# Optimization experiments

Measured on AMD Instinct MI355X. Metric: run time of the kernel, lower is better.

The kernel has to match this reference:

```python
import jax, jax.numpy as jnp
import numpy as np

NEG = -1e9
TAU = 1.0
N_SAMPLES = 5
SWEEP = (0.1, 0.5, 5)


def layer_norm(x, g, b, eps=1e-5):
    m = x.mean(-1, keepdims=True)
    v = x.var(-1, keepdims=True)
    return (x - m) / jnp.sqrt(v + eps) * g + b


def entmax15(z):
    # exact 1.5-entmax along last axis (Peters & Martins 2019 sort-based algorithm)
    z = z / 2.0
    zs = jnp.sort(z, axis=-1)[..., ::-1]               # descending
    T = z.shape[-1]
    kk = jnp.arange(1, T + 1, dtype=z.dtype)
    mean = jnp.cumsum(zs, -1) / kk
    mean_sq = jnp.cumsum(zs * zs, -1) / kk
    ss = kk * (mean_sq - mean * mean)
    delta = jnp.clip((1.0 - ss) / kk, 0.0)
    tau = mean - jnp.sqrt(delta)
    support = jnp.sum((tau <= zs).astype(jnp.int32), -1, keepdims=True)  # k_star
    tau_star = jnp.take_along_axis(tau, support - 1, axis=-1)
    return jnp.square(jnp.clip(z - tau_star, 0.0))


def stochastic_topk(key, scores, attn, k, tau, n_samples):
    # vectorized over samples AND batch rows with per-row variable k:
    # threshold = k-th largest perturbed score per row (ties measure-zero w/ gumbel)
    u = jax.random.uniform(key, (n_samples,) + scores.shape)
    noise = -jnp.log(-jnp.log(u + 1e-6) + 1e-6)
    pert = jnp.where(attn[None] == 0, NEG, scores[None] + noise * tau)  # [S,B,T]
    srt = jnp.sort(pert, -1)[..., ::-1]
    idx = jnp.broadcast_to((k - 1)[None, :, None], pert.shape[:2] + (1,))
    thr = jnp.take_along_axis(srt, idx, axis=-1)       # [S,B,1]
    h = (pert >= thr).astype(scores.dtype)
    return h.mean(0)                                   # [B,T]


def pool(tok, attn):
    # masked mean pooling (stand-in for sent_encoder.pool)
    return (tok * attn[..., None]).sum(1) / jnp.clip(attn.sum(1, keepdims=True), 1e-6)


def _forward(ids, embeddings, attn, ln_g, ln_b, W1, b1, W2, b2, emb_table):
    emb = embeddings * attn[..., None]
    h = jax.nn.gelu(layer_norm(emb, ln_g, ln_b) @ W1 + b1, approximate=False)
    scores = (h @ W2 + b2)[..., 0]                     # [B,T]
    scores = jnp.where(attn == 0, NEG, scores)

    tok = emb_table[ids]                               # stand-in token embeddings
    full_rep = jax.lax.stop_gradient(pool(tok, attn))  # torch.no_grad path

    T_eff = attn.sum(1)                                # [B]
    # g_soft is identical across the rho sweep in the original; hoisted here
    g_soft = entmax15(scores / TAU) * attn
    g_soft = g_soft / jnp.clip(g_soft.sum(1, keepdims=True), 1e-6)

    key = jax.random.key(42)
    rhos = np.linspace(*SWEEP)
    g_sweep, loss_sweep, rho_eff_sweep = [], [], []
    recon_sum = jnp.zeros((), embeddings.dtype)
    g = None
    for j, rho in enumerate(rhos):
        k = jnp.maximum((float(rho) * T_eff).astype(jnp.int32), 1)
        g_hard = stochastic_topk(jax.random.fold_in(key, j), scores, attn, k, TAU, N_SAMPLES)
        # straight-through: hard forward, soft (entmax) backward
        g = jax.lax.stop_gradient(g_hard) - jax.lax.stop_gradient(g_soft) + g_soft
        rho_eff_sweep.append(g.sum(1) / T_eff)
        eff_attn = attn * g
        pred_rep = pool(tok, eff_attn)
        l_r = jnp.mean(jnp.square(pred_rep - full_rep))  # recon_loss = MSE stand-in
        recon_sum = recon_sum + l_r
        g_sweep.append(g)
        loss_sweep.append(l_r)
    recon_avg = recon_sum / len(rhos)
    return g, jnp.stack(g_sweep), recon_avg, jnp.stack(loss_sweep), jnp.stack(rho_eff_sweep)


def setup_inputs() -> dict:
    key = jax.random.key(0)
    B, T, D, H, V = 8, 2048, 1024, 1365, 32000
    ks = jax.random.split(key, 8)
    return {
        "ids": jax.random.randint(ks[0], (B, T), 0, V),
        "embeddings": jax.random.normal(ks[1], (B, T, D), jnp.float32),
        "attn": jnp.ones((B, T), jnp.float32),
        "ln_g": jnp.ones((D,), jnp.float32),
        "ln_b": jnp.zeros((D,), jnp.float32),
        "W1": jax.random.normal(ks[2], (D, H), jnp.float32) * 0.02,
        "b1": jnp.zeros((H,), jnp.float32),
        "W2": jax.random.normal(ks[3], (H, 1), jnp.float32) * 0.02,
        "b2": jnp.zeros((1,), jnp.float32),
        "emb_table": jax.random.normal(ks[4], (V, D), jnp.float32) * 0.02,
    }


def reference(ids, embeddings, attn, ln_g, ln_b, W1, b1, W2, b2, emb_table):
    return _forward(ids, embeddings, attn, ln_g, ln_b, W1, b1, W2, b2, emb_table)
```

## Files before the change

kernel.cpp:

```cpp
#include <hip/hip_runtime.h>
#include <math.h>
#include <stdint.h>

#define B_ 8
#define T_ 2048
#define D_ 1024
#define H_ 1365
#define HPAD 1536
#define NTOK (B_*T_)
#define NSAMP 5
#define NRHO 5

typedef float  f32x4  __attribute__((ext_vector_type(4)));
typedef __bf16 bf16x8 __attribute__((ext_vector_type(8)));

#define WS_SCORES 0
#define WS_CNT    (WS_SCORES + NTOK*8)
#define WS_PREDW  (WS_CNT + NRHO*B_*T_*4)
#define WS_FULLW  (WS_PREDW + NRHO*B_*D_*8)
#define WS_SUMEFF (WS_FULLW + B_*D_*8)
#define WS_SUMATT (WS_SUMEFF + NRHO*B_*8)
#define WS_SUMG   (WS_SUMATT + B_*8)
#define WS_ZERO_BYTES (WS_SUMG + NRHO*B_*8)
#define WS_STATS  (WS_SUMG + NRHO*B_*8)
#define WS_W1THI  (WS_STATS + NTOK*8)
#define WS_W1TLO  (WS_W1THI + (size_t)HPAD*D_*2)
#define WS_AHI    (WS_W1TLO + (size_t)HPAD*D_*2)
#define WS_ALO    (WS_AHI + (size_t)NTOK*D_*2)
#define WS_FULL_END (WS_ALO + (size_t)NTOK*D_*2)

#define OUT_G      0
#define OUT_GSW    16384
#define OUT_RECON  98304
#define OUT_LOSS   98305
#define OUT_RHOEFF 98310

__device__ inline unsigned short f2bf(float x) {
    uint32_t u = __float_as_uint(x);
    return (unsigned short)((u + 0x7FFFu + ((u >> 16) & 1u)) >> 16);
}

__launch_bounds__(256)
__global__ void k_w1t(const float* __restrict__ W1, unsigned short* __restrict__ hi,
                      unsigned short* __restrict__ lo)
{
    __shared__ float tile[32][33];
    const int tid = threadIdx.x;
    const int bk = blockIdx.x & 31;
    const int bh = blockIdx.x >> 5;
    const int k0 = bk * 32, h0 = bh * 32;
    const int a = tid & 31, b = tid >> 5;
    #pragma unroll
    for (int i = 0; i < 4; ++i) {
        int k = k0 + b + i * 8;
        int h = h0 + a;
        tile[b + i*8][a] = (h < H_) ? W1[(size_t)k * H_ + h] : 0.0f;
    }
    __syncthreads();
    #pragma unroll
    for (int i = 0; i < 4; ++i) {
        int hrow = h0 + b + i * 8;
        int kcol = k0 + a;
        float v = tile[a][b + i*8];
        unsigned short hb = f2bf(v);
        float hf = __uint_as_float((uint32_t)hb << 16);
        unsigned short lb = f2bf(v - hf);
        size_t dst = (size_t)hrow * D_ + kcol;
        hi[dst] = hb; lo[dst] = lb;
    }
}

__launch_bounds__(256)
__global__ void k_asplit(const float* __restrict__ emb, const float* __restrict__ attn,
                         const float* __restrict__ ln_g, const float* __restrict__ ln_b,
                         unsigned short* __restrict__ ahi, unsigned short* __restrict__ alo)
{
    const int tid = threadIdx.x, l = tid & 63, w = tid >> 6;
    const int t0 = blockIdx.x * 64;
    for (int tk = w; tk < 64; tk += 4) {
        const int tg = t0 + tk;
        const float av = attn[tg];
        const float* row = emb + (size_t)tg * D_;
        float rv[16];
        double s1 = 0.0, s2 = 0.0;
        #pragma unroll
        for (int i = 0; i < 16; ++i) {
            rv[i] = row[i*64 + l];
            double x = (double)rv[i] * (double)av;
            s1 += x; s2 += x * x;
        }
        for (int m = 32; m; m >>= 1) { s1 += __shfl_xor(s1, m); s2 += __shfl_xor(s2, m); }
        double mean = s1 / (double)D_;
        double var  = s2 / (double)D_ - mean * mean;
        double inv  = 1.0 / sqrt(var + 1e-5);
        float sc  = (float)((double)av * inv);
        float nsh = -(float)(mean * inv);
        #pragma unroll
        for (int i = 0; i < 16; ++i) {
            int k = i * 64 + l;
            float t  = fmaf(rv[i], sc, nsh);
            float xn = fmaf(t, ln_g[k], ln_b[k]);
            unsigned short hb = f2bf(xn);
            float hf = __uint_as_float((uint32_t)hb << 16);
            size_t dst = (size_t)tg * D_ + k;
            ahi[dst] = hb;
            alo[dst] = f2bf(xn - hf);
        }
    }
}

__launch_bounds__(256)
__global__ void k_stats(const float* __restrict__ emb, const float* __restrict__ attn,
                        float2* __restrict__ stats)
{
    const int tid = threadIdx.x, l = tid & 63, w = tid >> 6;
    const int t0 = blockIdx.x * 64;
    for (int tk = w; tk < 64; tk += 4) {
        const int tg = t0 + tk;
        const float av = attn[tg];
        const float* row = emb + (size_t)tg * D_;
        double s1 = 0.0, s2 = 0.0;
        #pragma unroll
        for (int i = 0; i < D_/64; ++i) {
            double x = (double)row[i*64 + l] * (double)av;
            s1 += x; s2 += x * x;
        }
        for (int m = 32; m; m >>= 1) { s1 += __shfl_xor(s1, m); s2 += __shfl_xor(s2, m); }
        if (l == 0) {
            double mean = s1 / (double)D_;
            double var  = s2 / (double)D_ - mean * mean;
            double inv  = 1.0 / sqrt(var + 1e-5);
            stats[tg] = make_float2((float)((double)av * inv), (float)(mean * inv));
        }
    }
}

#define BUFU 24576
#define OFF_ALO 4096
#define OFF_BHI 8192
#define OFF_BLO 16384
#define KSTEPS 32

__device__ __forceinline__ void gll16(const unsigned short* g, unsigned short* l)
{
    __builtin_amdgcn_global_load_lds((const __attribute__((address_space(1))) void*)g,
                                     (__attribute__((address_space(3))) void*)l, 16, 0, 0);
}

__launch_bounds__(512, 2)
__global__ void k_scores8(const unsigned short* __restrict__ ahi,
                          const unsigned short* __restrict__ alo,
                          const unsigned short* __restrict__ w1thi,
                          const unsigned short* __restrict__ w1tlo,
                          const float* __restrict__ b1, const float* __restrict__ W2,
                          double* __restrict__ scores)
{
    __shared__ __align__(16) unsigned short smem[3*BUFU];

    const int tid = threadIdx.x;
    const int blk = blockIdx.x;
    const int lin = (blk & 7) * 96 + (blk >> 3);
    const int mm = lin / 6, hh = lin - mm * 6;
    const int t0 = mm * 128;
    const int h0 = hh * 256;

    const int l  = tid & 63, w = tid >> 6;
    const int wr = w >> 2, wcn = w & 3;
    const int lm = l & 15, lq = l >> 4;

    const int lrow  = l >> 2;
    const int lslot = (l & 3) ^ ((l >> 3) & 3);
    const unsigned short* sA_hi  = ahi   + (size_t)(t0 + w*16 + lrow) * D_ + lslot*8;
    const unsigned short* sA_lo  = alo   + (size_t)(t0 + w*16 + lrow) * D_ + lslot*8;
    const unsigned short* sB_hi0 = w1thi + (size_t)(h0 + w*32 + lrow) * D_ + lslot*8;
    const unsigned short* sB_hi1 = sB_hi0 + 16*D_;
    const unsigned short* sB_lo0 = w1tlo + (size_t)(h0 + w*32 + lrow) * D_ + lslot*8;
    const unsigned short* sB_lo1 = sB_lo0 + 16*D_;
    const int dAhi  = w*512,            dAlo  = OFF_ALO + w*512;
    const int dBhi0 = OFF_BHI + w*1024, dBhi1 = dBhi0 + 512;
    const int dBlo0 = OFF_BLO + w*1024, dBlo1 = dBlo0 + 512;

    const int sw8 = (lq ^ ((lm >> 1) & 3)) * 8;
    int offAh[4], offBh[4];
    #pragma unroll
    for (int r = 0; r < 4; ++r) offAh[r] = (wr*64 + r*16 + lm)*32 + sw8;
    #pragma unroll
    for (int c = 0; c < 4; ++c) offBh[c] = OFF_BHI + (wcn*64 + c*16 + lm)*32 + sw8;

    f32x4 acc[4][4];
    #pragma unroll
    for (int r = 0; r < 4; ++r)
        #pragma unroll
        for (int c = 0; c < 4; ++c) acc[r][c] = (f32x4){0.f, 0.f, 0.f, 0.f};

    gll16(sA_hi,       &smem[0*BUFU + dAhi]);
    gll16(sA_lo,       &smem[0*BUFU + dAlo]);
    gll16(sB_hi0,      &smem[0*BUFU + dBhi0]);
    gll16(sB_hi1,      &smem[0*BUFU + dBhi1]);
    gll16(sB_lo0,      &smem[0*BUFU + dBlo0]);
    gll16(sB_lo1,      &smem[0*BUFU + dBlo1]);
    gll16(sA_hi  + 32, &smem[1*BUFU + dAhi]);
    gll16(sA_lo  + 32, &smem[1*BUFU + dAlo]);
    gll16(sB_hi0 + 32, &smem[1*BUFU + dBhi0]);
    gll16(sB_hi1 + 32, &smem[1*BUFU + dBhi1]);
    gll16(sB_lo0 + 32, &smem[1*BUFU + dBlo0]);
    gll16(sB_lo1 + 32, &smem[1*BUFU + dBlo1]);
    asm volatile("s_waitcnt vmcnt(6)" ::: "memory");
    asm volatile("s_barrier" ::: "memory");

    int dbase = 0, ebase = 2*BUFU;
    #pragma unroll 1
    for (int t = 0; t < KSTEPS; ++t) {
        const int  stK = (t + 2) * 32;
        const bool st  = (t < KSTEPS - 2);
        bf16x8 ah[4], bh[4];
        #pragma unroll
        for (int r = 0; r < 4; ++r) ah[r] = *(const bf16x8*)&smem[dbase + offAh[r]];
        #pragma unroll
        for (int c = 0; c < 4; ++c) bh[c] = *(const bf16x8*)&smem[dbase + offBh[c]];
        if (st) { gll16(sA_hi + stK, &smem[ebase + dAhi]);
                  gll16(sA_lo + stK, &smem[ebase + dAlo]); }
        asm volatile("s_barrier" ::: "memory");
        asm volatile("s_waitcnt lgkmcnt(0)" ::: "memory");
        __builtin_amdgcn_sched_barrier(0);
        __builtin_amdgcn_s_setprio(1);
        #pragma unroll
        for (int r = 0; r < 4; ++r)
            #pragma unroll
            for (int c = 0; c < 4; ++c)
                acc[r][c] = __builtin_amdgcn_mfma_f32_16x16x32_bf16(ah[r], bh[c], acc[r][c], 0, 0, 0);
        __builtin_amdgcn_s_setprio(0);
        asm volatile("s_barrier" ::: "memory");
        bf16x8 bl[4];
        #pragma unroll
        for (int c = 0; c < 4; ++c) bl[c] = *(const bf16x8*)&smem[dbase + offBh[c] + (OFF_BLO - OFF_BHI)];
        if (st) { gll16(sB_hi0 + stK, &smem[ebase + dBhi0]);
                  gll16(sB_hi1 + stK, &smem[ebase + dBhi1]); }
        asm volatile("s_barrier" ::: "memory");
        asm volatile("s_waitcnt lgkmcnt(0)" ::: "memory");
        __builtin_amdgcn_sched_barrier(0);
        __builtin_amdgcn_s_setprio(1);
        #pragma unroll
        for (int r = 0; r < 4; ++r)
            #pragma unroll
            for (int c = 0; c < 4; ++c)
                acc[r][c] = __builtin_amdgcn_mfma_f32_16x16x32_bf16(ah[r], bl[c], acc[r][c], 0, 0, 0);
        __builtin_amdgcn_s_setprio(0);
        asm volatile("s_barrier" ::: "memory");
        bf16x8 al[4];
        #pragma unroll
        for (int r = 0; r < 4; ++r) al[r] = *(const bf16x8*)&smem[dbase + offAh[r] + OFF_ALO];
        if (st) { gll16(sB_lo0 + stK, &smem[ebase + dBlo0]);
                  gll16(sB_lo1 + stK, &smem[ebase + dBlo1]); }
        asm volatile("s_barrier" ::: "memory");
        asm volatile("s_waitcnt lgkmcnt(0)" ::: "memory");
        __builtin_amdgcn_sched_barrier(0);
        __builtin_amdgcn_s_setprio(1);
        #pragma unroll
        for (int r = 0; r < 4; ++r)
            #pragma unroll
            for (int c = 0; c < 4; ++c)
                acc[r][c] = __builtin_amdgcn_mfma_f32_16x16x32_bf16(al[r], bh[c], acc[r][c], 0, 0, 0);
        __builtin_amdgcn_s_setprio(0);
        if (st) asm volatile("s_waitcnt vmcnt(6)" ::: "memory");
        else    asm volatile("s_waitcnt vmcnt(0)" ::: "memory");
        asm volatile("s_barrier" ::: "memory");
        dbase = (dbase == 2*BUFU) ? 0 : dbase + BUFU;
        ebase = (ebase == 2*BUFU) ? 0 : ebase + BUFU;
    }

    float b1v[4], w2v[4];
    #pragma unroll
    for (int c = 0; c < 4; ++c) {
        int hg = h0 + wcn*64 + c*16 + lm;
        bool ok = (hg < H_);
        b1v[c] = ok ? b1[hg] : 0.0f;
        w2v[c] = ok ? W2[hg] : 0.0f;
    }
    const float is2 = 0.70710678118654752440f;
    #pragma unroll
    for (int r = 0; r < 4; ++r) {
        #pragma unroll
        for (int i = 0; i < 4; ++i) {
            float ps = 0.0f;
            #pragma unroll
            for (int c = 0; c < 4; ++c) {
                float z  = acc[r][c][i] + b1v[c];
                float gl = 0.5f * z * (1.0f + erff(z * is2));
                ps = fmaf(gl, w2v[c], ps);
            }
            double psd = (double)ps;
            psd += __shfl_xor(psd, 1);
            psd += __shfl_xor(psd, 2);
            psd += __shfl_xor(psd, 4);
            psd += __shfl_xor(psd, 8);
            if (lm == 0)
                atomicAdd(&scores[t0 + wr*64 + r*16 + lq*4 + i], psd);
        }
    }
}

__launch_bounds__(256)
__global__ void k_scores_fb(const float* __restrict__ emb, const float* __restrict__ ln_g,
                            const float* __restrict__ ln_b, const float2* __restrict__ stats,
                            const unsigned short* __restrict__ w1thi,
                            const unsigned short* __restrict__ w1tlo,
                            const float* __restrict__ b1, const float* __restrict__ W2,
                            double* __restrict__ scores)
{
    __shared__ __align__(16) unsigned short sAhi[128*40];
    __shared__ __align__(16) unsigned short sAlo[128*40];
    __shared__ __align__(16) unsigned short sBhi[128*40];
    __shared__ __align__(16) unsigned short sBlo[128*40];
    __shared__ float sS1[128], sS2[128];

    const int tid = threadIdx.x;
    const int blk = blockIdx.x;
    const int xcd = blk & 7, slot = blk >> 3;
    const int lin = xcd * 176 + slot;
    const int tt = lin / 11, hh = lin - tt * 11;
    const int t0 = tt * 128;
    const int h0 = hh * 128;

    if (tid < 128) {
        float2 st = stats[t0 + tid];
        sS1[tid] = st.x; sS2[tid] = st.y;
    }
    f32x4 acc[4][4];
    #pragma unroll
    for (int r = 0; r < 4; ++r)
        #pragma unroll
        for (int c = 0; c < 4; ++c) acc[r][c] = (f32x4){0.f, 0.f, 0.f, 0.f};
    const int l = tid & 63, w = tid >> 6;
    const int lm = l & 15, lq = l >> 4;
    const int wr = (w >> 1) * 64;
    const int wc = (w & 1) * 64;
    __syncthreads();

    for (int kc = 0; kc < D_; kc += 32) {
        #pragma unroll
        for (int r2 = 0; r2 < 2; ++r2) {
            int g = tid + r2 * 256;
            int row = g >> 2, oct = g & 3;
            size_t src = (size_t)(h0 + row) * D_ + kc + oct * 8;
            int dst = row * 40 + oct * 8;
            *(bf16x8*)&sBhi[dst] = *(const bf16x8*)&w1thi[src];
            *(bf16x8*)&sBlo[dst] = *(const bf16x8*)&w1tlo[src];
        }
        #pragma unroll
        for (int r2 = 0; r2 < 2; ++r2) {
            int g = tid + r2 * 256;
            int tk = g >> 2, oct = g & 3;
            int tg = t0 + tk, dg = kc + oct * 8;
            const float* ep = emb + (size_t)tg * D_ + dg;
            float s1 = sS1[tk], ns2 = -sS2[tk];
            union { unsigned short s[8]; bf16x8 v; } hi, lo;
            #pragma unroll
            for (int j = 0; j < 8; ++j) {
                float t  = fmaf(ep[j], s1, ns2);
                float xn = fmaf(t, ln_g[dg + j], ln_b[dg + j]);
                unsigned short hb = f2bf(xn);
                float hf = __uint_as_float((uint32_t)hb << 16);
                hi.s[j] = hb;
                lo.s[j] = f2bf(xn - hf);
            }
            int dst = tk * 40 + oct * 8;
            *(bf16x8*)&sAhi[dst] = hi.v;
            *(bf16x8*)&sAlo[dst] = lo.v;
        }
        __syncthreads();
        bf16x8 ah[4], al[4], bh[4], bl[4];
        #pragma unroll
        for (int r = 0; r < 4; ++r) {
            int off = (wr + r * 16 + lm) * 40 + lq * 8;
            ah[r] = *(const bf16x8*)&sAhi[off];
            al[r] = *(const bf16x8*)&sAlo[off];
        }
        #pragma unroll
        for (int c = 0; c < 4; ++c) {
            int off = (wc + c * 16 + lm) * 40 + lq * 8;
            bh[c] = *(const bf16x8*)&sBhi[off];
            bl[c] = *(const bf16x8*)&sBlo[off];
        }
        #pragma unroll
        for (int r = 0; r < 4; ++r)
            #pragma unroll
            for (int c = 0; c < 4; ++c) {
                acc[r][c] = __builtin_amdgcn_mfma_f32_16x16x32_bf16(ah[r], bh[c], acc[r][c], 0, 0, 0);
                acc[r][c] = __builtin_amdgcn_mfma_f32_16x16x32_bf16(ah[r], bl[c], acc[r][c], 0, 0, 0);
                acc[r][c] = __builtin_amdgcn_mfma_f32_16x16x32_bf16(al[r], bh[c], acc[r][c], 0, 0, 0);
            }
        __syncthreads();
    }
    float b1v[4], w2v[4];
    #pragma unroll
    for (int c = 0; c < 4; ++c) {
        int hg = h0 + wc + c * 16 + lm;
        bool ok = (hg < H_);
        b1v[c] = ok ? b1[hg] : 0.0f;
        w2v[c] = ok ? W2[hg] : 0.0f;
    }
    const float is2 = 0.70710678118654752440f;
    #pragma unroll
    for (int r = 0; r < 4; ++r) {
        #pragma unroll
        for (int i = 0; i < 4; ++i) {
            float ps = 0.0f;
            #pragma unroll
            for (int c = 0; c < 4; ++c) {
                float z  = acc[r][c][i] + b1v[c];
                float gl = 0.5f * z * (1.0f + erff(z * is2));
                ps = fmaf(gl, w2v[c], ps);
            }
            double psd = (double)ps;
            psd += __shfl_xor(psd, 1);
            psd += __shfl_xor(psd, 2);
            psd += __shfl_xor(psd, 4);
            psd += __shfl_xor(psd, 8);
            if (lm == 0)
                atomicAdd(&scores[t0 + wr + r * 16 + lq * 4 + i], psd);
        }
    }
}

__device__ inline void tf2x32(uint32_t k0, uint32_t k1, uint32_t x0, uint32_t x1,
                              uint32_t& o0, uint32_t& o1)
{
    const uint32_t ks2 = k0 ^ k1 ^ 0x1BD11BDAu;
    x0 += k0; x1 += k1;
#define ROT_(v,d) (((v) << (d)) | ((v) >> (32 - (d))))
#define RND_(R) { x0 += x1; x1 = ROT_(x1, R); x1 ^= x0; }
    RND_(13) RND_(15) RND_(26) RND_(6)
    x0 += k1;  x1 += ks2 + 1u;
    RND_(17) RND_(29) RND_(16) RND_(24)
    x0 += ks2; x1 += k0 + 2u;
    RND_(13) RND_(15) RND_(26) RND_(6)
    x0 += k0;  x1 += k1 + 3u;
    RND_(17) RND_(29) RND_(16) RND_(24)
    x0 += k1;  x1 += ks2 + 4u;
    RND_(13) RND_(15) RND_(26) RND_(6)
    x0 += ks2; x1 += k0 + 5u;
    o0 = x0; o1 = x1;
#undef RND_
#undef ROT_
}

__launch_bounds__(256)
__global__ void k_topk(const double* __restrict__ scores, const float* __restrict__ attn,
                       const float* __restrict__ b2, int* __restrict__ cnt)
{
    __shared__ unsigned long long keys[2048];
    __shared__ unsigned int hist[256];
    __shared__ unsigned int wsum[4];
    __shared__ unsigned int selDigit, selBase;
    __shared__ double red[4];

    const int tid = threadIdx.x;
    const int blk = blockIdx.x;
    const int j = blk / 40;
    const int s = (blk % 40) >> 3;
    const int b = blk & 7;

    uint32_t kk0, kk1;
    tf2x32(0u, 42u, 0u, (uint32_t)j, kk0, kk1);

    double tsum = 0.0;
    for (int t = tid; t < T_; t += 256) tsum += (double)attn[b * T_ + t];
    for (int m = 32; m; m >>= 1) tsum += __shfl_xor(tsum, m);
    if ((tid & 63) == 0) red[tid >> 6] = tsum;
    __syncthreads();
    const double Teff = red[0] + red[1] + red[2] + red[3];
    const float rhos[5] = {0.1f, 0.2f, 0.3f, 0.4f, 0.5f};
    int kst = (int)(rhos[j] * (float)Teff);
    if (kst < 1) kst = 1;

    const double bb2 = (double)b2[0];
    #pragma unroll
    for (int r = 0; r < 8; ++r) {
        int t = tid + r * 256;
        int f = (s * 8 + b) * T_ + t;
        uint32_t o0, o1;
        tf2x32(kk0, kk1, 0u, (uint32_t)f, o0, o1);
        uint32_t bits = o0 ^ o1;
        float u = __uint_as_float((bits >> 9) | 0x3f800000u) - 1.0f;
        float a1 = (float)((double)u + (double)1e-6f);
        float la = (float)log((double)a1);
        float m1 = (float)((double)1e-6f - (double)la);
        float lb = (float)log((double)m1);
        float noise = -lb;
        float av = attn[b * T_ + t];
        double pv = (av == 0.0f) ? -1e9 : (scores[b * T_ + t] + bb2 + (double)noise);
        unsigned long long uu = (unsigned long long)__double_as_longlong(pv);
        keys[t] = (uu >> 63) ? ~uu : (uu | 0x8000000000000000ull);
    }
    __syncthreads();

    unsigned long long pfx = 0;
    unsigned int plo = (unsigned int)(2048 - kst);
    const int lane = tid & 63, wv = tid >> 6;
    for (int pass = 0; pass < 8; ++pass) {
        const int shift = 56 - 8 * pass;
        const unsigned long long maskhi = (pass == 0) ? 0ull : (~0ull << (64 - 8 * pass));
        hist[tid] = 0;
        __syncthreads();
        #pragma unroll
        for (int r = 0; r < 8; ++r) {
            unsigned long long kk = keys[tid + r * 256];
            if ((kk & maskhi) == pfx)
                atomicAdd(&hist[(unsigned int)((kk >> shift) & 255ull)], 1u);
        }
        __syncthreads();
        unsigned int own = hist[tid];
        int val = (int)own;
        #pragma unroll
        for (int off = 1; off < 64; off <<= 1) {
            int n = __shfl_up(val, off);
            if (lane >= off) val += n;
        }
        if (lane == 63) wsum[wv] = (unsigned int)val;
        __syncthreads();
        unsigned int woff = 0;
        for (int q = 0; q < wv; ++q) woff += wsum[q];
        unsigned int incl = (unsigned int)val + woff;
        unsigned int excl = incl - own;
        if (own > 0 && plo >= excl && plo < incl) { selDigit = (unsigned int)tid; selBase = excl; }
        __syncthreads();
        pfx |= ((unsigned long long)selDigit << shift);
        plo -= selBase;
        __syncthreads();
    }

    #pragma unroll
    for (int r = 0; r < 8; ++r) {
        int t = tid + r * 256;
        if (keys[t] >= pfx) atomicAdd(&cnt[(j * 8 + b) * T_ + t], 1);
    }
}

__launch_bounds__(256)
__global__ void k_gfin(const int* __restrict__ cnt, const float* __restrict__ attn,
                       float* __restrict__ out, double* __restrict__ sumeff,
                       double* __restrict__ sumatt, double* __restrict__ sumg)
{
    __shared__ double redA[4], redB[4], redC[4];
    const int j = blockIdx.x >> 3, b = blockIdx.x & 7;
    const int tid = threadIdx.x;
    double sg = 0.0, se = 0.0, sa = 0.0;
    for (int t = tid; t < T_; t += 256) {
        int c = cnt[(j * 8 + b) * T_ + t];
        float g  = (float)c / 5.0f;
        float av = attn[b * T_ + t];
        out[OUT_GSW + (j * 8 + b) * T_ + t] = g;
        if (j == 4) out[OUT_G + b * T_ + t] = g;
        sg += (double)g;
        se += (double)(av * g);
        sa += (double)av;
    }
    for (int m = 32; m; m >>= 1) { sg += __shfl_xor(sg, m); se += __shfl_xor(se, m); sa += __shfl_xor(sa, m); }
    if ((tid & 63) == 0) { redA[tid>>6] = sg; redB[tid>>6] = se; redC[tid>>6] = sa; }
    __syncthreads();
    if (tid == 0) {
        sg = redA[0]+redA[1]+redA[2]+redA[3];
        se = redB[0]+redB[1]+redB[2]+redB[3];
        sa = redC[0]+redC[1]+redC[2]+redC[3];
        sumg[j*8+b] = sg; sumeff[j*8+b] = se;
        if (j == 0) sumatt[b] = sa;
        out[OUT_RHOEFF + j*8 + b] = (float)sg / (float)sa;
    }
}

__launch_bounds__(256)
__global__ void k_pool(const int* __restrict__ ids, const float* __restrict__ attn,
                       const float* __restrict__ out, const float* __restrict__ emb_table,
                       double* __restrict__ predw, double* __restrict__ fullw)
{
    __shared__ int   sid[128];
    __shared__ float sw[6][128];
    const int blk = blockIdx.x;
    const int b  = blk >> 6;
    const int dc = (blk >> 4) & 3;
    const int tc = blk & 15;
    const int tid = threadIdx.x;
    const int d = dc * 256 + tid;
    if (tid < 128) {
        int t = tc * 128 + tid;
        sid[tid] = ids[b * T_ + t];
        float av = attn[b * T_ + t];
        sw[0][tid] = av;
        #pragma unroll
        for (int j = 0; j < 5; ++j) {
            float g = out[OUT_GSW + (j * 8 + b) * T_ + t];
            sw[1 + j][tid] = av * g;
        }
    }
    __syncthreads();
    double acc[6] = {0,0,0,0,0,0};
    for (int i = 0; i < 128; ++i) {
        float val = emb_table[(size_t)sid[i] * D_ + d];
        #pragma unroll
        for (int c = 0; c < 6; ++c) acc[c] += (double)(val * sw[c][i]);
    }
    atomicAdd(&fullw[b * D_ + d], acc[0]);
    #pragma unroll
    for (int j = 0; j < 5; ++j)
        atomicAdd(&predw[(j * 8 + b) * D_ + d], acc[1 + j]);
}

__launch_bounds__(256)
__global__ void k_loss(const double* __restrict__ predw, const double* __restrict__ fullw,
                       const double* __restrict__ sumeff, const double* __restrict__ sumatt,
                       float* __restrict__ out)
{
    __shared__ double red[4];
    __shared__ float lr[5];
    const int tid = threadIdx.x;
    for (int j = 0; j < 5; ++j) {
        double p = 0.0;
        for (int i = tid; i < B_ * D_; i += 256) {
            int b = i >> 10;
            double dF = sumatt[b];        if (dF < 1e-6) dF = 1e-6;
            double dE = sumeff[j*8 + b];  if (dE < 1e-6) dE = 1e-6;
            double diff = predw[j * B_ * D_ + i] / dE - fullw[i] / dF;
            p += diff * diff;
        }
        for (int m = 32; m; m >>= 1) p += __shfl_xor(p, m);
        if ((tid & 63) == 0) red[tid >> 6] = p;
        __syncthreads();
        if (tid == 0) {
            double t = red[0] + red[1] + red[2] + red[3];
            lr[j] = (float)(t / (double)(B_ * D_));
            out[OUT_LOSS + j] = lr[j];
        }
        __syncthreads();
    }
    if (tid == 0) {
        float srec = 0.0f;
        for (int j = 0; j < 5; ++j) srec += lr[j];
        out[OUT_RECON] = srec / 5.0f;
    }
}

extern "C" void kernel_launch(void* const* d_in, const int* in_sizes, int n_in,
                              void* d_out, int out_size, void* d_ws, size_t ws_size,
                              hipStream_t stream)
{
    const int*   ids  = (const int*)  d_in[0];
    const float* emb  = (const float*)d_in[1];
    const float* attn = (const float*)d_in[2];
    const float* ln_g = (const float*)d_in[3];
    const float* ln_b = (const float*)d_in[4];
    const float* W1   = (const float*)d_in[5];
    const float* b1   = (const float*)d_in[6];
    const float* W2   = (const float*)d_in[7];
    const float* b2   = (const float*)d_in[8];
    const float* et   = (const float*)d_in[9];
    float* out = (float*)d_out;
    char*  ws  = (char*)d_ws;

    double* scores = (double*)(ws + WS_SCORES);
    int*    cnt    = (int*)   (ws + WS_CNT);
    double* predw  = (double*)(ws + WS_PREDW);
    double* fullw  = (double*)(ws + WS_FULLW);
    double* sumeff = (double*)(ws + WS_SUMEFF);
    double* sumatt = (double*)(ws + WS_SUMATT);
    double* sumg   = (double*)(ws + WS_SUMG);
    float2* stats  = (float2*)(ws + WS_STATS);
    unsigned short* w1thi = (unsigned short*)(ws + WS_W1THI);
    unsigned short* w1tlo = (unsigned short*)(ws + WS_W1TLO);
    unsigned short* ahi   = (unsigned short*)(ws + WS_AHI);
    unsigned short* alo   = (unsigned short*)(ws + WS_ALO);

    hipMemsetAsync(d_ws, 0, WS_ZERO_BYTES, stream);

    k_w1t<<<48*32, 256, 0, stream>>>(W1, w1thi, w1tlo);
    if (ws_size >= WS_FULL_END) {
        k_asplit<<<NTOK/64, 256, 0, stream>>>(emb, attn, ln_g, ln_b, ahi, alo);
        k_scores8<<<768, 512, 0, stream>>>(ahi, alo, w1thi, w1tlo, b1, W2, scores);
    } else {
        k_stats<<<NTOK/64, 256, 0, stream>>>(emb, attn, stats);
        k_scores_fb<<<1408, 256, 0, stream>>>(emb, ln_g, ln_b, stats, w1thi, w1tlo,
                                              b1, W2, scores);
    }
    k_topk<<<NRHO * NSAMP * B_, 256, 0, stream>>>(scores, attn, b2, cnt);
    k_gfin<<<NRHO * B_, 256, 0, stream>>>(cnt, attn, out, sumeff, sumatt, sumg);
    k_pool<<<512, 256, 0, stream>>>(ids, attn, out, et, predw, fullw);
    k_loss<<<1, 256, 0, stream>>>(predw, fullw, sumeff, sumatt, out);
}
```

Baseline: 502.0 us.

## Fully unroll GEMM K-loop and collapse per-phase barriers into one per step

Result: no change. 495.9 us (-1.2%).

```diff
diff --git a/kernel.cpp b/kernel.cpp
--- a/kernel.cpp
+++ b/kernel.cpp
@@ -208,65 +208,48 @@
     asm volatile("s_waitcnt vmcnt(6)" ::: "memory");
     asm volatile("s_barrier" ::: "memory");
 
-    int dbase = 0, ebase = 2*BUFU;
-    #pragma unroll 1
+    #pragma unroll
     for (int t = 0; t < KSTEPS; ++t) {
-        const int  stK = (t + 2) * 32;
-        const bool st  = (t < KSTEPS - 2);
-        bf16x8 ah[4], bh[4];
+        const int dbase = (t % 3) * BUFU;
+        const int ebase = ((t + 2) % 3) * BUFU;
+        const int stK   = (t + 2) * 32;
+        if (t < KSTEPS - 2) {
+            gll16(sA_hi  + stK, &smem[ebase + dAhi]);
+            gll16(sA_lo  + stK, &smem[ebase + dAlo]);
+            gll16(sB_hi0 + stK, &smem[ebase + dBhi0]);
+            gll16(sB_hi1 + stK, &smem[ebase + dBhi1]);
+            gll16(sB_lo0 + stK, &smem[ebase + dBlo0]);
+            gll16(sB_lo1 + stK, &smem[ebase + dBlo1]);
+        }
+        bf16x8 ah[4], bh[4], bl[4], al[4];
         #pragma unroll
         for (int r = 0; r < 4; ++r) ah[r] = *(const bf16x8*)&smem[dbase + offAh[r]];
         #pragma unroll
         for (int c = 0; c < 4; ++c) bh[c] = *(const bf16x8*)&smem[dbase + offBh[c]];
-        if (st) { gll16(sA_hi + stK, &smem[ebase + dAhi]);
-                  gll16(sA_lo + stK, &smem[ebase + dAlo]); }
-        asm volatile("s_barrier" ::: "memory");
-        asm volatile("s_waitcnt lgkmcnt(0)" ::: "memory");
-        __builtin_amdgcn_sched_barrier(0);
         __builtin_amdgcn_s_setprio(1);
         #pragma unroll
         for (int r = 0; r < 4; ++r)
             #pragma unroll
             for (int c = 0; c < 4; ++c)
                 acc[r][c] = __builtin_amdgcn_mfma_f32_16x16x32_bf16(ah[r], bh[c], acc[r][c], 0, 0, 0);
-        __builtin_amdgcn_s_setprio(0);
-        asm volatile("s_barrier" ::: "memory");
-        bf16x8 bl[4];
         #pragma unroll
         for (int c = 0; c < 4; ++c) bl[c] = *(const bf16x8*)&smem[dbase + offBh[c] + (OFF_BLO - OFF_BHI)];
-        if (st) { gll16(sB_hi0 + stK, &smem[ebase + dBhi0]);
-                  gll16(sB_hi1 + stK, &smem[ebase + dBhi1]); }
-        asm volatile("s_barrier" ::: "memory");
-        asm volatile("s_waitcnt lgkmcnt(0)" ::: "memory");
-        __builtin_amdgcn_sched_barrier(0);
-        __builtin_amdgcn_s_setprio(1);
         #pragma unroll
         for (int r = 0; r < 4; ++r)
             #pragma unroll
             for (int c = 0; c < 4; ++c)
                 acc[r][c] = __builtin_amdgcn_mfma_f32_16x16x32_bf16(ah[r], bl[c], acc[r][c], 0, 0, 0);
-        __builtin_amdgcn_s_setprio(0);
-        asm volatile("s_barrier" ::: "memory");
-        bf16x8 al[4];
         #pragma unroll
         for (int r = 0; r < 4; ++r) al[r] = *(const bf16x8*)&smem[dbase + offAh[r] + OFF_ALO];
-        if (st) { gll16(sB_lo0 + stK, &smem[ebase + dBlo0]);
-                  gll16(sB_lo1 + stK, &smem[ebase + dBlo1]); }
-        asm volatile("s_barrier" ::: "memory");
-        asm volatile("s_waitcnt lgkmcnt(0)" ::: "memory");
-        __builtin_amdgcn_sched_barrier(0);
-        __builtin_amdgcn_s_setprio(1);
         #pragma unroll
         for (int r = 0; r < 4; ++r)
             #pragma unroll
             for (int c = 0; c < 4; ++c)
                 acc[r][c] = __builtin_amdgcn_mfma_f32_16x16x32_bf16(al[r], bh[c], acc[r][c], 0, 0, 0);
         __builtin_amdgcn_s_setprio(0);
-        if (st) asm volatile("s_waitcnt vmcnt(6)" ::: "memory");
-        else    asm volatile("s_waitcnt vmcnt(0)" ::: "memory");
-        asm volatile("s_barrier" ::: "memory");
-        dbase = (dbase == 2*BUFU) ? 0 : dbase + BUFU;
-        ebase = (ebase == 2*BUFU) ? 0 : ebase + BUFU;
+        if (t < KSTEPS - 2)       asm volatile("s_waitcnt vmcnt(6)" ::: "memory");
+        else if (t == KSTEPS - 2) asm volatile("s_waitcnt vmcnt(0)" ::: "memory");
+        if (t < KSTEPS - 1)       asm volatile("s_barrier" ::: "memory");
     }
 
     float b1v[4], w2v[4];
```
